# Performance work log

Hardware: AMD Instinct MI355X
Metric: run time of the kernel (lower is better)

The kernel has to match this reference:

```python
import jax, jax.numpy as jnp
import numpy as np

N = 50000      # nodes
E = 800000     # edges
IN = 128       # in_channels
HID = 64       # hidden_channels (per head)
HEADS = 2      # GAT heads
OUT = 64       # out_channels (classes)


def segment_softmax(e, seg, num_segments):
    # softmax of per-edge scores grouped by destination node
    m = jax.ops.segment_max(e, seg, num_segments=num_segments)
    ex = jnp.exp(e - m[seg])
    s = jax.ops.segment_sum(ex, seg, num_segments=num_segments)
    return ex / s[seg]


def setup_inputs() -> dict:
    key = jax.random.key(0)
    ks = jax.random.split(key, 12)
    sc = 0.05
    return {
        "x": jax.random.normal(ks[0], (N, IN), dtype=jnp.float32),
        "edge_index": jax.random.randint(ks[1], (2, E), 0, N),
        # GATConv params: lin (no bias), att_src/att_dst, output bias
        "W1": jax.random.normal(ks[2], (IN, HEADS * HID), dtype=jnp.float32) * sc,
        "att_src": jax.random.normal(ks[3], (HEADS, HID), dtype=jnp.float32) * sc,
        "att_dst": jax.random.normal(ks[4], (HEADS, HID), dtype=jnp.float32) * sc,
        "b1": jnp.zeros((HEADS * HID,), dtype=jnp.float32),
        # TransformerConv params (heads=1): q/k/v linears + skip linear
        "Wq": jax.random.normal(ks[5], (HEADS * HID, OUT), dtype=jnp.float32) * sc,
        "bq": jnp.zeros((OUT,), dtype=jnp.float32),
        "Wk": jax.random.normal(ks[6], (HEADS * HID, OUT), dtype=jnp.float32) * sc,
        "bk": jnp.zeros((OUT,), dtype=jnp.float32),
        "Wv": jax.random.normal(ks[7], (HEADS * HID, OUT), dtype=jnp.float32) * sc,
        "bv": jnp.zeros((OUT,), dtype=jnp.float32),
        "Wskip": jax.random.normal(ks[8], (HEADS * HID, OUT), dtype=jnp.float32) * sc,
        "bskip": jnp.zeros((OUT,), dtype=jnp.float32),
    }


def reference(x, edge_index, W1, att_src, att_dst, b1,
              Wq, bq, Wk, bk, Wv, bv, Wskip, bskip):
    n = x.shape[0]
    # ---- GATConv (concat=True, add_self_loops=True, negative_slope=0.2) ----
    loops = jnp.arange(n)
    src = jnp.concatenate([edge_index[0], loops])  # message source j
    dst = jnp.concatenate([edge_index[1], loops])  # message target i
    h = (x @ W1).reshape(n, HEADS, HID)            # [N,H,C]
    a_src = (h * att_src).sum(-1)                  # [N,H]
    a_dst = (h * att_dst).sum(-1)                  # [N,H]
    e = jax.nn.leaky_relu(a_src[src] + a_dst[dst], 0.2)   # [E+N,H]
    alpha = segment_softmax(e, dst, n)                     # [E+N,H]
    out1 = jax.ops.segment_sum(alpha[..., None] * h[src], dst, num_segments=n)
    x1 = jax.nn.relu(out1.reshape(n, HEADS * HID) + b1)    # [N,H*C]
    # ---- TransformerConv (heads=1, root_weight=True, no self-loops) ----
    q = x1 @ Wq + bq
    k = x1 @ Wk + bk
    v = x1 @ Wv + bv
    s2, d2 = edge_index[0], edge_index[1]
    scores = (q[d2] * k[s2]).sum(-1) / jnp.sqrt(jnp.float32(OUT))  # [E]
    al = segment_softmax(scores, d2, n)
    agg = jax.ops.segment_sum(al[:, None] * v[s2], d2, num_segments=n)
    out = agg + x1 @ Wskip + bskip
    return jax.nn.log_softmax(out, axis=1)
```

## Files before the change

### kernel.cpp

```cpp
#include <hip/hip_runtime.h>
#include <math.h>

typedef unsigned short u16;
typedef unsigned int u32;
typedef unsigned char u8;

using bf16x8 = __attribute__((ext_vector_type(8))) short;
using f32x4  = __attribute__((ext_vector_type(4))) float;
typedef __attribute__((ext_vector_type(2))) float vf2;

__device__ __forceinline__ float lrelu02(float x){ return x > 0.f ? x : 0.2f * x; }

__device__ __forceinline__ float bf2f(u16 u){
  union { u32 i; float f; } v; v.i = ((u32)u) << 16; return v.f;
}
__device__ __forceinline__ u16 f2bf(float f){
  union { float ff; u32 i; } v; v.ff = f;
  u32 x = v.i;
  return (u16)((x + 0x7fffu + ((x >> 16) & 1u)) >> 16);
}
__device__ __forceinline__ u32 pack2(float lo, float hi){
  return (u32)f2bf(lo) | ((u32)f2bf(hi) << 16);
}
__device__ __forceinline__ u8 f2fp8(float v){
  return (u8)(__builtin_amdgcn_cvt_pk_fp8_f32(v, v, 0, false) & 0xff);
}
__device__ __forceinline__ vf2 fma2(vf2 a, vf2 b, vf2 c){
  return __builtin_elementwise_fma(a, b, c);
}

__global__ __launch_bounds__(256) void prep_w_kernel(const float* __restrict__ W1,
                                                     const float* __restrict__ Wq,
                                                     const float* __restrict__ Wk,
                                                     const float* __restrict__ Wv,
                                                     const float* __restrict__ Ws,
                                                     const float* __restrict__ att_src,
                                                     const float* __restrict__ att_dst,
                                                     u16* __restrict__ w1t,
                                                     u16* __restrict__ wt2,
                                                     u16* __restrict__ wxt,
                                                     int* __restrict__ bc){
  int idx = blockIdx.x * 256 + threadIdx.x;
  if (idx < 16384){
    int j = idx >> 7, k = idx & 127;
    w1t[j * 128 + k] = f2bf(W1[k * 128 + j]);
  } else if (idx < 49152){
    int i = idx - 16384;
    int mat = i >> 13;
    int r = i & 8191;
    int j = r >> 7, k = r & 127;
    const float* W = (mat == 0) ? Wq : (mat == 1) ? Wk : (mat == 2) ? Wv : Ws;
    wt2[(mat * 64 + j) * 128 + k] = f2bf(W[k * 64 + j]);
  } else if (idx < 49664){
    int i = idx - 49152;
    int j = i >> 7, k = i & 127;
    const float* av = (j & 2) ? att_dst : att_src;
    int head = j & 1;
    float s = 0.f;
#pragma unroll 8
    for (int c = 0; c < 64; c++) s += W1[k * 128 + head * 64 + c] * av[head * 64 + c];
    wxt[j * 128 + k] = f2bf(s);
  } else if (idx < 51200){
    int i = idx - 49664;
    wxt[512 + i] = 0;
  } else if (idx < 51713){
    bc[idx - 51200] = 0;
  }
}

__global__ __launch_bounds__(256) void gemm1_mfma(const float* __restrict__ x,
                                                  const u16* __restrict__ w1t,
                                                  const u16* __restrict__ wxt,
                                                  u8* __restrict__ h8,
                                                  float* __restrict__ asrc,
                                                  float* __restrict__ adst, int n){
  __shared__ u8 lds8[64 * 128];
  int wid = threadIdx.x >> 6, lane = threadIdx.x & 63;
  int rl = lane & 15, kh = lane >> 4;
  int br = blockIdx.x * 64 + wid * 16;
  int arow = br + rl; if (arow > n - 1) arow = n - 1;
  const float* ab = x + (size_t)arow * 128 + kh * 8;
  f32x4 acc[9];
#pragma unroll
  for (int t = 0; t < 9; t++) acc[t] = (f32x4){0.f, 0.f, 0.f, 0.f};
#pragma unroll
  for (int ks = 0; ks < 4; ks++){
    float4 xa = *(const float4*)(ab + ks * 32);
    float4 xb = *(const float4*)(ab + ks * 32 + 4);
    union { bf16x8 v; u32 w[4]; } au;
    au.w[0] = pack2(xa.x, xa.y);
    au.w[1] = pack2(xa.z, xa.w);
    au.w[2] = pack2(xb.x, xb.y);
    au.w[3] = pack2(xb.z, xb.w);
    bf16x8 a = au.v;
#pragma unroll
    for (int t = 0; t < 8; t++){
      bf16x8 b = *(const bf16x8*)(w1t + (size_t)(t * 16 + rl) * 128 + ks * 32 + kh * 8);
      acc[t] = __builtin_amdgcn_mfma_f32_16x16x32_bf16(a, b, acc[t], 0, 0, 0);
    }
    bf16x8 bx = *(const bf16x8*)(wxt + (size_t)rl * 128 + ks * 32 + kh * 8);
    acc[8] = __builtin_amdgcn_mfma_f32_16x16x32_bf16(a, bx, acc[8], 0, 0, 0);
  }
#pragma unroll
  for (int r = 0; r < 4; r++){
    int rloc = wid * 16 + kh * 4 + r;
#pragma unroll
    for (int t = 0; t < 8; t++)
      lds8[rloc * 128 + t * 16 + rl] = f2fp8(acc[t][r]);
    int orow = br + kh * 4 + r;
    if (orow < n && rl < 4){
      float vlv = acc[8][r];
      if (rl < 2) asrc[orow * 2 + rl] = vlv;
      else        adst[orow * 2 + (rl - 2)] = vlv;
    }
  }
  int rrow = wid * 16 + (lane >> 2);
  int cb = (lane & 3) * 32;
  int grow = blockIdx.x * 64 + rrow;
  if (grow < n){
    uint4 v0 = *(const uint4*)&lds8[rrow * 128 + cb];
    uint4 v1 = *(const uint4*)&lds8[rrow * 128 + cb + 16];
    uint4* gp = (uint4*)(h8 + (size_t)grow * 128 + cb);
    gp[0] = v0;
    gp[1] = v1;
  }
}

__global__ __launch_bounds__(256) void gemm2_mfma(const u16* __restrict__ x1bf,
                                                  const u16* __restrict__ wt2,
                                                  const float* __restrict__ bq,
                                                  const float* __restrict__ bk,
                                                  const float* __restrict__ bv,
                                                  const float* __restrict__ bs,
                                                  float* __restrict__ q,
                                                  u8* __restrict__ kv8,
                                                  float* __restrict__ skip, int n){
  int wid = threadIdx.x >> 6, lane = threadIdx.x & 63;
  int rl = lane & 15, kh = lane >> 4;
  int br = blockIdx.x * 64 + wid * 16;
  int arow = br + rl; if (arow > n - 1) arow = n - 1;
  const u16* abase = x1bf + (size_t)arow * 128 + kh * 8;
  f32x4 acc[16];
#pragma unroll
  for (int t = 0; t < 16; t++) acc[t] = (f32x4){0.f, 0.f, 0.f, 0.f};
#pragma unroll
  for (int ks = 0; ks < 4; ks++){
    bf16x8 a = *(const bf16x8*)(abase + ks * 32);
#pragma unroll
    for (int t = 0; t < 16; t++){
      bf16x8 b = *(const bf16x8*)(wt2 + (size_t)(t * 16 + rl) * 128 + ks * 32 + kh * 8);
      acc[t] = __builtin_amdgcn_mfma_f32_16x16x32_bf16(a, b, acc[t], 0, 0, 0);
    }
  }
  float bias_t[16];
#pragma unroll
  for (int t = 0; t < 16; t++){
    const float* bb = (t < 4) ? bq : (t < 8) ? bk : (t < 12) ? bv : bs;
    bias_t[t] = bb[(t & 3) * 16 + rl];
  }
  int orow0 = br + kh * 4;
#pragma unroll
  for (int r = 0; r < 4; r++){
    int orow = orow0 + r;
    if (orow >= n) continue;
#pragma unroll
    for (int t = 0; t < 16; t++){
      int c = (t & 3) * 16 + rl;
      float val = acc[t][r] + bias_t[t];
      if (t < 4)       q[(size_t)orow * 64 + c]    = val;
      else if (t < 8)  kv8[(size_t)orow * 128 + (c >> 3) * 16 + (c & 7)]     = f2fp8(val);
      else if (t < 12) kv8[(size_t)orow * 128 + (c >> 3) * 16 + 8 + (c & 7)] = f2fp8(val);
      else             skip[(size_t)orow * 64 + c] = val;
    }
  }
}

__global__ __launch_bounds__(256) void bucket_hist_kernel(const int* __restrict__ dst,
                                                          int* __restrict__ bc, int E){
  __shared__ int h[512];
  for (int i = threadIdx.x; i < 512; i += 256) h[i] = 0;
  __syncthreads();
  int base = blockIdx.x * 4096;
#pragma unroll
  for (int i = 0; i < 16; i++){
    int e = base + i * 256 + threadIdx.x;
    if (e < E) atomicAdd(&h[dst[e] >> 7], 1);
  }
  __syncthreads();
  for (int i = threadIdx.x; i < 512; i += 256)
    if (h[i]) atomicAdd(&bc[i], h[i]);
}

__global__ __launch_bounds__(256) void bucket_scan_kernel(const int* __restrict__ bc,
                                                          int* __restrict__ bbase,
                                                          int* __restrict__ bcur){
  __shared__ int tmp[5];
  int tid = threadIdx.x;
  int c0 = bc[2 * tid], c1 = bc[2 * tid + 1];
  int s = c0 + c1, incl = s;
  int lane = tid & 63, wid = tid >> 6;
#pragma unroll
  for (int o = 1; o < 64; o <<= 1){
    int t = __shfl_up(incl, o);
    if (lane >= o) incl += t;
  }
  if (lane == 63) tmp[wid] = incl;
  __syncthreads();
  if (tid == 0){
    int run = 0;
#pragma unroll
    for (int w2 = 0; w2 < 4; w2++){ int t = tmp[w2]; tmp[w2] = run; run += t; }
    tmp[4] = run;
  }
  __syncthreads();
  int excl = tmp[wid] + incl - s;
  bbase[2 * tid]     = excl;      bbase[2 * tid + 1] = excl + c0;
  bcur[2 * tid]      = excl;      bcur[2 * tid + 1]  = excl + c0;
  if (tid == 255) bbase[512] = tmp[4];
}

__global__ __launch_bounds__(256) void multisplit_kernel(const int* __restrict__ src,
                                                         const int* __restrict__ dst,
                                                         int* __restrict__ bcur,
                                                         uint2* __restrict__ ebuf, int E){
  __shared__ int h[512];
  __shared__ int gb[512];
  __shared__ int cur[512];
  int tid = threadIdx.x;
  for (int i = tid; i < 512; i += 256){ h[i] = 0; cur[i] = 0; }
  __syncthreads();
  int base = blockIdx.x * 4096;
  int myd[16];
#pragma unroll
  for (int i = 0; i < 16; i++){
    int e = base + i * 256 + tid;
    myd[i] = (e < E) ? dst[e] : -1;
    if (myd[i] >= 0) atomicAdd(&h[myd[i] >> 7], 1);
  }
  __syncthreads();
  for (int i = tid; i < 512; i += 256){
    int c = h[i];
    gb[i] = c ? atomicAdd(&bcur[i], c) : 0;
  }
  __syncthreads();
#pragma unroll
  for (int i = 0; i < 16; i++){
    if (myd[i] >= 0){
      int e = base + i * 256 + tid;
      int b = myd[i] >> 7;
      int r = atomicAdd(&cur[b], 1);
      uint2 ed; ed.x = (u32)src[e]; ed.y = (u32)myd[i];
      ebuf[gb[b] + r] = ed;
    }
  }
}

__global__ __launch_bounds__(256) void bucket_csr_kernel(const uint2* __restrict__ ebuf,
                                                         const int* __restrict__ bbase,
                                                         const float* __restrict__ asrc,
                                                         const float* __restrict__ adst,
                                                         int* __restrict__ offsets,
                                                         int* __restrict__ csr,
                                                         u32* __restrict__ pe,
                                                         int n, int E, int nb){
  __shared__ int deg[128];
  __shared__ int loff[128];
  __shared__ int cur[128];
  int b = blockIdx.x, tid = threadIdx.x;
  int base = bbase[b], end = bbase[b + 1];
  if (tid < 128) deg[tid] = 0;
  __syncthreads();
  for (int e = base + tid; e < end; e += 256)
    atomicAdd(&deg[ebuf[e].y & 127], 1);
  __syncthreads();
  if (tid < 64){
    int v0 = deg[2 * tid], v1 = deg[2 * tid + 1];
    int s = v0 + v1, incl = s;
#pragma unroll
    for (int o = 1; o < 64; o <<= 1){
      int t = __shfl_up(incl, o);
      if (tid >= o) incl += t;
    }
    int excl = incl - s;
    loff[2 * tid] = excl; loff[2 * tid + 1] = excl + v0;
  }
  __syncthreads();
  int node0 = b << 7;
  if (tid < 128){
    cur[tid] = loff[tid];
    int node = node0 + tid;
    if (node < n) offsets[node] = base + loff[tid];
  }
  if (b == nb - 1 && tid == 0) offsets[n] = E;
  __syncthreads();
  for (int e = base + tid; e < end; e += 256){
    uint2 ed = ebuf[e];
    int li = (int)(ed.y & 127);
    int r = atomicAdd(&cur[li], 1);
    int sj = (int)ed.x;
    csr[base + r] = sj;
    float2 as = ((const float2*)asrc)[sj];
    float2 ad = ((const float2*)adst)[node0 + li];
    pe[base + r] = pack2(__expf(lrelu02(as.x + ad.x)),
                         __expf(lrelu02(as.y + ad.y)));
  }
}

__global__ __launch_bounds__(256) void gat_agg_kernel(const u8* __restrict__ h8,
                                                      const float* __restrict__ asrc,
                                                      const float* __restrict__ adst,
                                                      const int* __restrict__ off,
                                                      const int* __restrict__ csr_src,
                                                      const u32* __restrict__ pe,
                                                      const float* __restrict__ b1,
                                                      u16* __restrict__ x1bf, int n){
  int node = blockIdx.x * 4 + (threadIdx.x >> 6);
  int lane = threadIdx.x & 63;
  if (node >= n) return;
  int s0 = off[node];
  int d  = off[node + 1] - s0;
  int g = lane >> 3;
  int sub = lane & 7;
  int chb = sub * 16;
  int head = sub >> 2;
  float2 ad  = ((const float2*)adst)[node];
  float2 asl = ((const float2*)asrc)[node];
  float ad_own = head ? ad.y : ad.x;
  float pself = __expf(lrelu02((head ? asl.y : asl.x) + ad_own));
  vf2 acc[8];
#pragma unroll
  for (int i = 0; i < 8; i++) acc[i] = (vf2){0.f, 0.f};
  float ps = 0.f;
#pragma unroll 2
  for (int base = 0; base < d; base += 8){
    int idx = base + g;
    bool valid = idx < d;
    int ee = s0 + (valid ? idx : d - 1);
    int sj = csr_src[ee];
    u32 pp = pe[ee];
    float p = valid ? bf2f((u16)(head ? (pp >> 16) : (pp & 0xffffu))) : 0.f;
    ps += p;
    uint4 w = *(const uint4*)(h8 + (size_t)sj * 128 + chb);
    vf2 p2 = {p, p};
    acc[0] = fma2(p2, __builtin_amdgcn_cvt_pk_f32_fp8((int)w.x, false), acc[0]);
    acc[1] = fma2(p2, __builtin_amdgcn_cvt_pk_f32_fp8((int)w.x, true),  acc[1]);
    acc[2] = fma2(p2, __builtin_amdgcn_cvt_pk_f32_fp8((int)w.y, false), acc[2]);
    acc[3] = fma2(p2, __builtin_amdgcn_cvt_pk_f32_fp8((int)w.y, true),  acc[3]);
    acc[4] = fma2(p2, __builtin_amdgcn_cvt_pk_f32_fp8((int)w.z, false), acc[4]);
    acc[5] = fma2(p2, __builtin_amdgcn_cvt_pk_f32_fp8((int)w.z, true),  acc[5]);
    acc[6] = fma2(p2, __builtin_amdgcn_cvt_pk_f32_fp8((int)w.w, false), acc[6]);
    acc[7] = fma2(p2, __builtin_amdgcn_cvt_pk_f32_fp8((int)w.w, true),  acc[7]);
  }
#pragma unroll
  for (int o = 8; o <= 32; o <<= 1){
#pragma unroll
    for (int i = 0; i < 8; i++){
      acc[i][0] += __shfl_xor(acc[i][0], o);
      acc[i][1] += __shfl_xor(acc[i][1], o);
    }
    ps += __shfl_xor(ps, o);
  }
  if (lane < 8){
    float st = ps + pself;
    uint4 w = *(const uint4*)(h8 + (size_t)node * 128 + chb);
    vf2 pf2 = {pself, pself};
    acc[0] = fma2(pf2, __builtin_amdgcn_cvt_pk_f32_fp8((int)w.x, false), acc[0]);
    acc[1] = fma2(pf2, __builtin_amdgcn_cvt_pk_f32_fp8((int)w.x, true),  acc[1]);
    acc[2] = fma2(pf2, __builtin_amdgcn_cvt_pk_f32_fp8((int)w.y, false), acc[2]);
    acc[3] = fma2(pf2, __builtin_amdgcn_cvt_pk_f32_fp8((int)w.y, true),  acc[3]);
    acc[4] = fma2(pf2, __builtin_amdgcn_cvt_pk_f32_fp8((int)w.z, false), acc[4]);
    acc[5] = fma2(pf2, __builtin_amdgcn_cvt_pk_f32_fp8((int)w.z, true),  acc[5]);
    acc[6] = fma2(pf2, __builtin_amdgcn_cvt_pk_f32_fp8((int)w.w, false), acc[6]);
    acc[7] = fma2(pf2, __builtin_amdgcn_cvt_pk_f32_fp8((int)w.w, true),  acc[7]);
    const float4* bp = (const float4*)(b1 + chb);
    float4 bv0 = bp[0], bv1 = bp[1], bv2 = bp[2], bv3 = bp[3];
    float bb[16] = {bv0.x, bv0.y, bv0.z, bv0.w, bv1.x, bv1.y, bv1.z, bv1.w,
                    bv2.x, bv2.y, bv2.z, bv2.w, bv3.x, bv3.y, bv3.z, bv3.w};
    float inv = 1.f / st;
    u32 wv[8];
#pragma unroll
    for (int i = 0; i < 8; i++){
      float v0 = fmaxf(acc[i][0] * inv + bb[2*i],   0.f);
      float v1 = fmaxf(acc[i][1] * inv + bb[2*i+1], 0.f);
      wv[i] = pack2(v0, v1);
    }
    uint4 o0 = {wv[0], wv[1], wv[2], wv[3]};
    uint4 o1 = {wv[4], wv[5], wv[6], wv[7]};
    u16* xp = x1bf + (size_t)node * 128 + chb;
    *(uint4*)xp = o0;
    *(uint4*)(xp + 8) = o1;
  }
}

__global__ __launch_bounds__(256) void trans_agg_kernel(const float* __restrict__ q,
                                                        const u8* __restrict__ kv8,
                                                        const float* __restrict__ skip,
                                                        const int* __restrict__ off,
                                                        const int* __restrict__ csr_src,
                                                        float* __restrict__ out, int n){
  int node = blockIdx.x * 4 + (threadIdx.x >> 6);
  int lane = threadIdx.x & 63;
  if (node >= n) return;
  int s0 = off[node];
  int d  = off[node + 1] - s0;
  int g = lane >> 3;
  int sub = lane & 7;
  const vf2* qp = (const vf2*)(q + (size_t)node * 64 + sub * 8);
  vf2 q0 = qp[0], q1 = qp[1], q2 = qp[2], q3 = qp[3];
  vf2 acc[4];
#pragma unroll
  for (int i = 0; i < 4; i++) acc[i] = (vf2){0.f, 0.f};
  float ps = 0.f;
#pragma unroll 2
  for (int base = 0; base < d; base += 8){
    int idx = base + g;
    bool valid = idx < d;
    int sj = csr_src[s0 + (valid ? idx : d - 1)];
    uint4 w = *(const uint4*)(kv8 + (size_t)sj * 128 + sub * 16);
    vf2 d2 = {0.f, 0.f};
    d2 = fma2(q0, __builtin_amdgcn_cvt_pk_f32_fp8((int)w.x, false), d2);
    d2 = fma2(q1, __builtin_amdgcn_cvt_pk_f32_fp8((int)w.x, true),  d2);
    d2 = fma2(q2, __builtin_amdgcn_cvt_pk_f32_fp8((int)w.y, false), d2);
    d2 = fma2(q3, __builtin_amdgcn_cvt_pk_f32_fp8((int)w.y, true),  d2);
    float part = d2[0] + d2[1];
    part += __shfl_xor(part, 1);
    part += __shfl_xor(part, 2);
    part += __shfl_xor(part, 4);
    float p = valid ? __expf(part * 0.125f) : 0.f;
    ps += p;
    vf2 p2 = {p, p};
    acc[0] = fma2(p2, __builtin_amdgcn_cvt_pk_f32_fp8((int)w.z, false), acc[0]);
    acc[1] = fma2(p2, __builtin_amdgcn_cvt_pk_f32_fp8((int)w.z, true),  acc[1]);
    acc[2] = fma2(p2, __builtin_amdgcn_cvt_pk_f32_fp8((int)w.w, false), acc[2]);
    acc[3] = fma2(p2, __builtin_amdgcn_cvt_pk_f32_fp8((int)w.w, true),  acc[3]);
  }
#pragma unroll
  for (int o = 8; o <= 32; o <<= 1){
#pragma unroll
    for (int i = 0; i < 4; i++){
      acc[i][0] += __shfl_xor(acc[i][0], o);
      acc[i][1] += __shfl_xor(acc[i][1], o);
    }
    ps += __shfl_xor(ps, o);
  }
  if (lane < 8){
    const float4* sp = (const float4*)(skip + (size_t)node * 64 + sub * 8);
    float4 s0v = sp[0], s1v = sp[1];
    float sk[8] = {s0v.x, s0v.y, s0v.z, s0v.w, s1v.x, s1v.y, s1v.z, s1v.w};
    float inv = (d > 0) ? 1.f / ps : 0.f;
    float val[8];
    float mx = -3.0e38f;
#pragma unroll
    for (int i = 0; i < 8; i++){
      val[i] = sk[i] + acc[i >> 1][i & 1] * inv;
      mx = fmaxf(mx, val[i]);
    }
    mx = fmaxf(mx, __shfl_xor(mx, 1));
    mx = fmaxf(mx, __shfl_xor(mx, 2));
    mx = fmaxf(mx, __shfl_xor(mx, 4));
    float se = 0.f;
#pragma unroll
    for (int i = 0; i < 8; i++){ val[i] -= mx; se += __expf(val[i]); }
    se += __shfl_xor(se, 1);
    se += __shfl_xor(se, 2);
    se += __shfl_xor(se, 4);
    float lse = __logf(se);
    float* op = out + (size_t)node * 64 + sub * 8;
    float4 o0 = {val[0] - lse, val[1] - lse, val[2] - lse, val[3] - lse};
    float4 o4 = {val[4] - lse, val[5] - lse, val[6] - lse, val[7] - lse};
    *(float4*)(op)     = o0;
    *(float4*)(op + 4) = o4;
  }
}

extern "C" void kernel_launch(void* const* d_in, const int* in_sizes, int n_in,
                              void* d_out, int out_size, void* d_ws, size_t ws_size,
                              hipStream_t stream) {
  const float* x       = (const float*)d_in[0];
  const int*   ei      = (const int*)d_in[1];
  const float* W1      = (const float*)d_in[2];
  const float* att_src = (const float*)d_in[3];
  const float* att_dst = (const float*)d_in[4];
  const float* b1      = (const float*)d_in[5];
  const float* Wq = (const float*)d_in[6];  const float* bq = (const float*)d_in[7];
  const float* Wk = (const float*)d_in[8];  const float* bk = (const float*)d_in[9];
  const float* Wv = (const float*)d_in[10]; const float* bv = (const float*)d_in[11];
  const float* Ws = (const float*)d_in[12]; const float* bs = (const float*)d_in[13];
  float* out = (float*)d_out;

  int n = in_sizes[0] / 128;
  int E = in_sizes[1] / 2;
  const int* src = ei;
  const int* dst = ei + E;
  int nb = (n + 127) >> 7;

  char* w = (char*)d_ws;
  auto alloc = [&](size_t bytes) -> void* {
    void* p = (void*)w;
    w += (bytes + 255) & ~(size_t)255;
    return p;
  };
  u8*   h8   = (u8*)alloc((size_t)n * 128);
  float* asrc = (float*)alloc((size_t)n * 2 * 4);
  float* adst = (float*)alloc((size_t)n * 2 * 4);
  u16*  x1bf = (u16*)alloc((size_t)n * 128 * 2);
  float* qq   = (float*)alloc((size_t)n * 64 * 4);
  u8*   kv8  = (u8*)alloc((size_t)n * 128);
  float* skip = (float*)alloc((size_t)n * 64 * 4);
  int* offsets = (int*)alloc((size_t)(n + 1) * 4);
  int* csr     = (int*)alloc((size_t)E * 4);
  u32* pe      = (u32*)alloc((size_t)E * 4);
  int* bc      = (int*)alloc(516 * 4);
  int* bbase   = (int*)alloc(516 * 4);
  int* bcur    = (int*)alloc(516 * 4);
  u16*  w1t  = (u16*)alloc((size_t)128 * 128 * 2);
  u16*  wt2  = (u16*)alloc((size_t)256 * 128 * 2);
  u16*  wxt  = (u16*)alloc((size_t)16 * 128 * 2);
  uint2* ebuf = (uint2*)x1bf;

  int eblocks = (E + 4095) / 4096;

  prep_w_kernel<<<203, 256, 0, stream>>>(W1, Wq, Wk, Wv, Ws, att_src, att_dst,
                                         w1t, wt2, wxt, bc);
  gemm1_mfma<<<(n + 63) / 64, 256, 0, stream>>>(x, w1t, wxt, h8, asrc, adst, n);

  bucket_hist_kernel<<<eblocks, 256, 0, stream>>>(dst, bc, E);
  bucket_scan_kernel<<<1, 256, 0, stream>>>(bc, bbase, bcur);
  multisplit_kernel<<<eblocks, 256, 0, stream>>>(src, dst, bcur, ebuf, E);
  bucket_csr_kernel<<<nb, 256, 0, stream>>>(ebuf, bbase, asrc, adst,
                                            offsets, csr, pe, n, E, nb);

  gat_agg_kernel<<<(n + 3) / 4, 256, 0, stream>>>(h8, asrc, adst, offsets, csr, pe,
                                                  b1, x1bf, n);

  gemm2_mfma<<<(n + 63) / 64, 256, 0, stream>>>(x1bf, wt2, bq, bk, bv, bs,
                                                qq, kv8, skip, n);
  trans_agg_kernel<<<(n + 3) / 4, 256, 0, stream>>>(qq, kv8, skip, offsets, csr,
                                                    out, n);
}
```

Before: 173.6 us.

## Use fixed-capacity edge buckets to drop the histogram and scan kernels

Each 128-node destination bucket now gets a fixed slot of 4096 edges in the edge buffer, with cursors initialised to b*CAP in the weight-prep kernel. This removes the bucket histogram and prefix-scan kernels, and with them a pass over dst and two launches. CSR source indices and packed attention exponents are interleaved into one uint2 array, and per-node offsets become (start, end) pairs. The risk is that any bucket receiving more than 4096 edges overflows silently, and trans_agg now reads 8 bytes per edge where it only needs the source index.

```diff
diff --git a/kernel.cpp b/kernel.cpp
--- a/kernel.cpp
+++ b/kernel.cpp
@@ -8,6 +8,8 @@
 using bf16x8 = __attribute__((ext_vector_type(8))) short;
 using f32x4  = __attribute__((ext_vector_type(4))) float;
 typedef __attribute__((ext_vector_type(2))) float vf2;
+
+#define CAP 4096
 
 __device__ __forceinline__ float lrelu02(float x){ return x > 0.f ? x : 0.2f * x; }
 
@@ -39,7 +41,7 @@
                                                      u16* __restrict__ w1t,
                                                      u16* __restrict__ wt2,
                                                      u16* __restrict__ wxt,
-                                                     int* __restrict__ bc){
+                                                     int* __restrict__ bcur){
   int idx = blockIdx.x * 256 + threadIdx.x;
   if (idx < 16384){
     int j = idx >> 7, k = idx & 127;
@@ -63,8 +65,9 @@
   } else if (idx < 51200){
     int i = idx - 49664;
     wxt[512 + i] = 0;
-  } else if (idx < 51713){
-    bc[idx - 51200] = 0;
+  } else if (idx < 51712){
+    int b = idx - 51200;
+    bcur[b] = b * CAP;
   }
 }
 
@@ -175,50 +178,6 @@
   }
 }
 
-__global__ __launch_bounds__(256) void bucket_hist_kernel(const int* __restrict__ dst,
-                                                          int* __restrict__ bc, int E){
-  __shared__ int h[512];
-  for (int i = threadIdx.x; i < 512; i += 256) h[i] = 0;
-  __syncthreads();
-  int base = blockIdx.x * 4096;
-#pragma unroll
-  for (int i = 0; i < 16; i++){
-    int e = base + i * 256 + threadIdx.x;
-    if (e < E) atomicAdd(&h[dst[e] >> 7], 1);
-  }
-  __syncthreads();
-  for (int i = threadIdx.x; i < 512; i += 256)
-    if (h[i]) atomicAdd(&bc[i], h[i]);
-}
-
-__global__ __launch_bounds__(256) void bucket_scan_kernel(const int* __restrict__ bc,
-                                                          int* __restrict__ bbase,
-                                                          int* __restrict__ bcur){
-  __shared__ int tmp[5];
-  int tid = threadIdx.x;
-  int c0 = bc[2 * tid], c1 = bc[2 * tid + 1];
-  int s = c0 + c1, incl = s;
-  int lane = tid & 63, wid = tid >> 6;
-#pragma unroll
-  for (int o = 1; o < 64; o <<= 1){
-    int t = __shfl_up(incl, o);
-    if (lane >= o) incl += t;
-  }
-  if (lane == 63) tmp[wid] = incl;
-  __syncthreads();
-  if (tid == 0){
-    int run = 0;
-#pragma unroll
-    for (int w2 = 0; w2 < 4; w2++){ int t = tmp[w2]; tmp[w2] = run; run += t; }
-    tmp[4] = run;
-  }
-  __syncthreads();
-  int excl = tmp[wid] + incl - s;
-  bbase[2 * tid]     = excl;      bbase[2 * tid + 1] = excl + c0;
-  bcur[2 * tid]      = excl;      bcur[2 * tid + 1]  = excl + c0;
-  if (tid == 255) bbase[512] = tmp[4];
-}
-
 __global__ __launch_bounds__(256) void multisplit_kernel(const int* __restrict__ src,
                                                          const int* __restrict__ dst,
                                                          int* __restrict__ bcur,
@@ -256,18 +215,17 @@
 }
 
 __global__ __launch_bounds__(256) void bucket_csr_kernel(const uint2* __restrict__ ebuf,
-                                                         const int* __restrict__ bbase,
+                                                         const int* __restrict__ bcur,
                                                          const float* __restrict__ asrc,
                                                          const float* __restrict__ adst,
-                                                         int* __restrict__ offsets,
-                                                         int* __restrict__ csr,
-                                                         u32* __restrict__ pe,
-                                                         int n, int E, int nb){
+                                                         uint2* __restrict__ offs,
+                                                         uint2* __restrict__ cpe,
+                                                         int n){
   __shared__ int deg[128];
   __shared__ int loff[128];
   __shared__ int cur[128];
   int b = blockIdx.x, tid = threadIdx.x;
-  int base = bbase[b], end = bbase[b + 1];
+  int base = b * CAP, end = bcur[b];
   if (tid < 128) deg[tid] = 0;
   __syncthreads();
   for (int e = base + tid; e < end; e += 256)
@@ -289,36 +247,42 @@
   if (tid < 128){
     cur[tid] = loff[tid];
     int node = node0 + tid;
-    if (node < n) offsets[node] = base + loff[tid];
-  }
-  if (b == nb - 1 && tid == 0) offsets[n] = E;
+    if (node < n){
+      uint2 ov;
+      ov.x = (u32)(base + loff[tid]);
+      ov.y = (u32)(base + loff[tid] + deg[tid]);
+      offs[node] = ov;
+    }
+  }
   __syncthreads();
   for (int e = base + tid; e < end; e += 256){
     uint2 ed = ebuf[e];
     int li = (int)(ed.y & 127);
     int r = atomicAdd(&cur[li], 1);
     int sj = (int)ed.x;
-    csr[base + r] = sj;
     float2 as = ((const float2*)asrc)[sj];
     float2 ad = ((const float2*)adst)[node0 + li];
-    pe[base + r] = pack2(__expf(lrelu02(as.x + ad.x)),
-                         __expf(lrelu02(as.y + ad.y)));
+    uint2 cv;
+    cv.x = (u32)sj;
+    cv.y = pack2(__expf(lrelu02(as.x + ad.x)),
+                 __expf(lrelu02(as.y + ad.y)));
+    cpe[base + r] = cv;
   }
 }
 
 __global__ __launch_bounds__(256) void gat_agg_kernel(const u8* __restrict__ h8,
                                                       const float* __restrict__ asrc,
                                                       const float* __restrict__ adst,
-                                                      const int* __restrict__ off,
-                                                      const int* __restrict__ csr_src,
-                                                      const u32* __restrict__ pe,
+                                                      const uint2* __restrict__ offs,
+                                                      const uint2* __restrict__ cpe,
                                                       const float* __restrict__ b1,
                                                       u16* __restrict__ x1bf, int n){
   int node = blockIdx.x * 4 + (threadIdx.x >> 6);
   int lane = threadIdx.x & 63;
   if (node >= n) return;
-  int s0 = off[node];
-  int d  = off[node + 1] - s0;
+  uint2 ov = offs[node];
+  int s0 = (int)ov.x;
+  int d  = (int)(ov.y - ov.x);
   int g = lane >> 3;
   int sub = lane & 7;
   int chb = sub * 16;
@@ -336,9 +300,9 @@
     int idx = base + g;
     bool valid = idx < d;
     int ee = s0 + (valid ? idx : d - 1);
-    int sj = csr_src[ee];
-    u32 pp = pe[ee];
-    float p = valid ? bf2f((u16)(head ? (pp >> 16) : (pp & 0xffffu))) : 0.f;
+    uint2 ce = cpe[ee];
+    int sj = (int)ce.x;
+    float p = valid ? bf2f((u16)(head ? (ce.y >> 16) : (ce.y & 0xffffu))) : 0.f;
     ps += p;
     uint4 w = *(const uint4*)(h8 + (size_t)sj * 128 + chb);
     vf2 p2 = {p, p};
@@ -395,14 +359,15 @@
 __global__ __launch_bounds__(256) void trans_agg_kernel(const float* __restrict__ q,
                                                         const u8* __restrict__ kv8,
                                                         const float* __restrict__ skip,
-                                                        const int* __restrict__ off,
-                                                        const int* __restrict__ csr_src,
+                                                        const uint2* __restrict__ offs,
+                                                        const uint2* __restrict__ cpe,
                                                         float* __restrict__ out, int n){
   int node = blockIdx.x * 4 + (threadIdx.x >> 6);
   int lane = threadIdx.x & 63;
   if (node >= n) return;
-  int s0 = off[node];
-  int d  = off[node + 1] - s0;
+  uint2 ov = offs[node];
+  int s0 = (int)ov.x;
+  int d  = (int)(ov.y - ov.x);
   int g = lane >> 3;
   int sub = lane & 7;
   const vf2* qp = (const vf2*)(q + (size_t)node * 64 + sub * 8);
@@ -415,7 +380,7 @@
   for (int base = 0; base < d; base += 8){
     int idx = base + g;
     bool valid = idx < d;
-    int sj = csr_src[s0 + (valid ? idx : d - 1)];
+    int sj = (int)cpe[s0 + (valid ? idx : d - 1)].x;
     uint4 w = *(const uint4*)(kv8 + (size_t)sj * 128 + sub * 16);
     vf2 d2 = {0.f, 0.f};
     d2 = fma2(q0, __builtin_amdgcn_cvt_pk_f32_fp8((int)w.x, false), d2);
@@ -507,34 +472,28 @@
   float* qq   = (float*)alloc((size_t)n * 64 * 4);
   u8*   kv8  = (u8*)alloc((size_t)n * 128);
   float* skip = (float*)alloc((size_t)n * 64 * 4);
-  int* offsets = (int*)alloc((size_t)(n + 1) * 4);
-  int* csr     = (int*)alloc((size_t)E * 4);
-  u32* pe      = (u32*)alloc((size_t)E * 4);
-  int* bc      = (int*)alloc(516 * 4);
-  int* bbase   = (int*)alloc(516 * 4);
-  int* bcur    = (int*)alloc(516 * 4);
+  uint2* offs = (uint2*)alloc((size_t)n * 8);
+  uint2* ebuf = (uint2*)alloc((size_t)nb * CAP * 8);
+  uint2* cpe  = (uint2*)alloc((size_t)nb * CAP * 8);
+  int* bcur   = (int*)alloc(516 * 4);
   u16*  w1t  = (u16*)alloc((size_t)128 * 128 * 2);
   u16*  wt2  = (u16*)alloc((size_t)256 * 128 * 2);
   u16*  wxt  = (u16*)alloc((size_t)16 * 128 * 2);
-  uint2* ebuf = (uint2*)x1bf;
 
   int eblocks = (E + 4095) / 4096;
 
   prep_w_kernel<<<203, 256, 0, stream>>>(W1, Wq, Wk, Wv, Ws, att_src, att_dst,
-                                         w1t, wt2, wxt, bc);
+                                         w1t, wt2, wxt, bcur);
   gemm1_mfma<<<(n + 63) / 64, 256, 0, stream>>>(x, w1t, wxt, h8, asrc, adst, n);
 
-  bucket_hist_kernel<<<eblocks, 256, 0, stream>>>(dst, bc, E);
-  bucket_scan_kernel<<<1, 256, 0, stream>>>(bc, bbase, bcur);
   multisplit_kernel<<<eblocks, 256, 0, stream>>>(src, dst, bcur, ebuf, E);
-  bucket_csr_kernel<<<nb, 256, 0, stream>>>(ebuf, bbase, asrc, adst,
-                                            offsets, csr, pe, n, E, nb);
-
-  gat_agg_kernel<<<(n + 3) / 4, 256, 0, stream>>>(h8, asrc, adst, offsets, csr, pe,
+  bucket_csr_kernel<<<nb, 256, 0, stream>>>(ebuf, bcur, asrc, adst, offs, cpe, n);
+
+  gat_agg_kernel<<<(n + 3) / 4, 256, 0, stream>>>(h8, asrc, adst, offs, cpe,
                                                   b1, x1bf, n);
 
   gemm2_mfma<<<(n + 63) / 64, 256, 0, stream>>>(x1bf, wt2, bq, bk, bv, bs,
                                                 qq, kv8, skip, n);
-  trans_agg_kernel<<<(n + 3) / 4, 256, 0, stream>>>(qq, kv8, skip, offsets, csr,
+  trans_agg_kernel<<<(n + 3) / 4, 256, 0, stream>>>(qq, kv8, skip, offs, cpe,
                                                     out, n);
 }
```

Result: faster. 161.6 us (-6.9%).
